# Performance work log

Measured on AMD Instinct MI355X. Metric: run time of the kernel, lower is better.

Reference implementation:

```python
import jax, jax.numpy as jnp
import numpy as np

N_NODES = 500_000
N_EDGES = 32_000_000

def setup_inputs() -> dict:
    key = jax.random.key(0)
    k1, k2, k3 = jax.random.split(key, 3)
    x = jax.random.uniform(k1, (N_NODES, 1), dtype=jnp.float32)
    edge_index = jax.random.randint(k2, (2, N_EDGES), 0, N_NODES, dtype=jnp.int32)
    edge_probs = jax.random.uniform(k3, (N_EDGES,), dtype=jnp.float32)
    edge_weight = jnp.ones((1,), dtype=jnp.float32)
    self_loop = jnp.ones((1,), dtype=jnp.float32)
    return {"x": x, "edge_index": edge_index, "edge_probs": edge_probs,
            "edge_weight": edge_weight, "self_loop": self_loop}

def reference(x, edge_index, edge_probs, edge_weight, self_loop):
    # x: (N,1), edge_index: (2,E), edge_probs: (E,)
    src = edge_index[0]
    dst = edge_index[1]
    # messages: (E,1) = 1 - x[src] * p_e * w
    messages = 1.0 - x[src] * edge_probs[:, None] * edge_weight
    # scatter-multiply into dst nodes; nodes with no incoming edges get 1
    agg = jax.ops.segment_prod(messages, dst, num_segments=x.shape[0])
    return agg + self_loop * x
```

## Files before the change

kernel.cpp:

```cpp
#include <hip/hip_runtime.h>


#if defined(__has_builtin) && __has_builtin(__builtin_amdgcn_exp2f)
#define EXP2F(v) __builtin_amdgcn_exp2f(v)
#else
#define EXP2F(v) exp2f(v)
#endif

#define BLK 256
#define NB_SHIFT 13
#define NB (1 << NB_SHIFT)
#define EPB 16384
#define MAXK 256

__device__ __forceinline__ unsigned xcc_id() {
    return __builtin_amdgcn_s_getreg((31 << 11) | 20) & 7u;
}
__device__ __forceinline__ void atomic_fadd_l2(float* p, float v) {
    asm volatile("global_atomic_add_f32 %0, %1, off" :: "v"(p), "v"(v) : "memory");
}
__device__ __forceinline__ void atomic_fadd_agent(float* p, float v) {
    unsafeAtomicAdd(p, v);
}

__global__ void init_zero(float* __restrict__ ws, int n) {
    int i = blockIdx.x * blockDim.x + threadIdx.x;
    if (i < n) ws[i] = 0.0f;
}

template <bool USE_L2>
__global__ __launch_bounds__(256) void edge_scatter(
        const float* __restrict__ x,
        const int* __restrict__ src,
        const int* __restrict__ dst,
        const float* __restrict__ probs,
        const float* __restrict__ w_ptr,
        float* __restrict__ logsum,
        int n_nodes, int n_e4) {
    const float w = w_ptr[0];
    float* ls = USE_L2 ? (logsum + (size_t)xcc_id() * (size_t)n_nodes) : logsum;
    int i = blockIdx.x * blockDim.x + threadIdx.x;
    if (i >= n_e4) return;
    int4   s = ((const int4*)src)[i];
    int4   d = ((const int4*)dst)[i];
    float4 p = ((const float4*)probs)[i];
    float m0 = __log2f(1.0f - x[s.x] * p.x * w);
    float m1 = __log2f(1.0f - x[s.y] * p.y * w);
    float m2 = __log2f(1.0f - x[s.z] * p.z * w);
    float m3 = __log2f(1.0f - x[s.w] * p.w * w);
    if (USE_L2) {
        atomic_fadd_l2(&ls[d.x], m0); atomic_fadd_l2(&ls[d.y], m1);
        atomic_fadd_l2(&ls[d.z], m2); atomic_fadd_l2(&ls[d.w], m3);
    } else {
        atomic_fadd_agent(&ls[d.x], m0); atomic_fadd_agent(&ls[d.y], m1);
        atomic_fadd_agent(&ls[d.z], m2); atomic_fadd_agent(&ls[d.w], m3);
    }
}

template <bool USE_L2>
__global__ void edge_scatter_tail(
        const float* __restrict__ x,
        const int* __restrict__ src,
        const int* __restrict__ dst,
        const float* __restrict__ probs,
        const float* __restrict__ w_ptr,
        float* __restrict__ logsum,
        int n_nodes, int start, int n_edges) {
    const float w = w_ptr[0];
    float* ls = USE_L2 ? (logsum + (size_t)xcc_id() * (size_t)n_nodes) : logsum;
    int i = start + blockIdx.x * blockDim.x + threadIdx.x;
    if (i >= n_edges) return;
    float m = __log2f(1.0f - x[src[i]] * probs[i] * w);
    if (USE_L2) atomic_fadd_l2(&ls[dst[i]], m);
    else        atomic_fadd_agent(&ls[dst[i]], m);
}

__global__ void finalize8(const float* __restrict__ x,
                          const float* __restrict__ sl_ptr,
                          const float* __restrict__ logsum,
                          float* __restrict__ out, int n) {
    int i = blockIdx.x * blockDim.x + threadIdx.x;
    if (i >= n) return;
    float s = 0.0f;
    #pragma unroll
    for (int r = 0; r < 8; ++r) s += logsum[(size_t)r * n + i];
    out[i] = EXP2F(s) + sl_ptr[0] * x[i];
}

__global__ void finalize1(const float* __restrict__ x,
                          const float* __restrict__ sl_ptr,
                          const float* __restrict__ logsum,
                          float* __restrict__ out, int n) {
    int i = blockIdx.x * blockDim.x + threadIdx.x;
    if (i < n) out[i] = EXP2F(logsum[i]) + sl_ptr[0] * x[i];
}


__global__ __launch_bounds__(256) void k_hist(
        const int* __restrict__ dstp,
        unsigned* __restrict__ hist,
        int ebase, int ecount, int K, int G0, int vec_ok) {
    __shared__ unsigned h[MAXK];
    const int b = blockIdx.x;
    const int t = threadIdx.x;
    for (int i = t; i < K; i += BLK) h[i] = 0;
    __syncthreads();
    const int begin = ebase + b * EPB;
    const int end   = min(begin + EPB, ebase + ecount);
    if (vec_ok) {
        for (int e0 = begin + t * 4; e0 < end; e0 += BLK * 4) {
            if (e0 + 4 <= end) {
                const int4 d = *(const int4*)(dstp + e0);
                atomicAdd(&h[(unsigned)d.x >> NB_SHIFT], 1u);
                atomicAdd(&h[(unsigned)d.y >> NB_SHIFT], 1u);
                atomicAdd(&h[(unsigned)d.z >> NB_SHIFT], 1u);
                atomicAdd(&h[(unsigned)d.w >> NB_SHIFT], 1u);
            } else {
                for (int e = e0; e < end; ++e)
                    atomicAdd(&h[(unsigned)dstp[e] >> NB_SHIFT], 1u);
            }
        }
    } else {
        for (int e0 = begin + t * 4; e0 < end; e0 += BLK * 4) {
            const int ee = min(e0 + 4, end);
            for (int e = e0; e < ee; ++e)
                atomicAdd(&h[(unsigned)dstp[e] >> NB_SHIFT], 1u);
        }
    }
    __syncthreads();
    for (int i = t; i < K; i += BLK) hist[(size_t)i * G0 + b] = h[i];
}

__global__ __launch_bounds__(256) void k_scan_row(
        unsigned* __restrict__ hist, unsigned* __restrict__ btot,
        int G0, int Gr) {
    __shared__ unsigned wsum[4];
    __shared__ unsigned carry;
    const int k = blockIdx.x;
    const int t = threadIdx.x;
    unsigned* row = hist + (size_t)k * G0;
    if (t == 0) carry = 0;
    __syncthreads();
    for (int c0 = 0; c0 < Gr; c0 += BLK) {
        const unsigned v = (c0 + t < Gr) ? row[c0 + t] : 0u;
        unsigned xs = v;
        #pragma unroll
        for (int o = 1; o < 64; o <<= 1) {
            const unsigned y = __shfl_up(xs, o, 64);
            if ((t & 63) >= o) xs += y;
        }
        if ((t & 63) == 63) wsum[t >> 6] = xs;
        __syncthreads();
        unsigned woff = 0;
        for (int wv = 0; wv < (t >> 6); ++wv) woff += wsum[wv];
        const unsigned ex = xs + woff - v + carry;
        if (c0 + t < Gr) row[c0 + t] = ex;
        const unsigned ctot = wsum[0] + wsum[1] + wsum[2] + wsum[3];
        __syncthreads();
        if (t == 0) carry += ctot;
        __syncthreads();
    }
    if (t == 0) btot[k] = carry;
}

__global__ __launch_bounds__(256) void k_scan_bkt(
        const unsigned* __restrict__ btot, unsigned* __restrict__ bbase, int K) {
    __shared__ unsigned wsum[4];
    const int t = threadIdx.x;
    const unsigned v = (t < K) ? btot[t] : 0u;
    unsigned xs = v;
    #pragma unroll
    for (int o = 1; o < 64; o <<= 1) {
        const unsigned y = __shfl_up(xs, o, 64);
        if ((t & 63) >= o) xs += y;
    }
    if ((t & 63) == 63) wsum[t >> 6] = xs;
    __syncthreads();
    unsigned woff = 0;
    for (int wv = 0; wv < (t >> 6); ++wv) woff += wsum[wv];
    if (t < K) bbase[t] = xs + woff - v;
}

__global__ __launch_bounds__(256) void k_scatter(
        const float* __restrict__ x,
        const int* __restrict__ src,
        const int* __restrict__ dstp,
        const float* __restrict__ probs,
        const float* __restrict__ w_ptr,
        const unsigned* __restrict__ base,
        const unsigned* __restrict__ bbase,
        uint2* __restrict__ queue,
        int ebase, int ecount, int K, int G0, int vec_ok) {
    __shared__ unsigned cur[MAXK];
    const int b = blockIdx.x;
    const int t = threadIdx.x;
    for (int i = t; i < K; i += BLK)
        cur[i] = bbase[i] + base[(size_t)i * G0 + b];
    __syncthreads();
    const float w = w_ptr[0];
    const int begin = ebase + b * EPB;
    const int end   = min(begin + EPB, ebase + ecount);
    auto one = [&](int e) {
        const int dv = dstp[e];
        const float m = __log2f(1.0f - x[src[e]] * probs[e] * w);
        const unsigned kk = (unsigned)dv >> NB_SHIFT;
        const unsigned r = atomicAdd(&cur[kk], 1u);
        queue[r] = make_uint2((unsigned)dv & (NB - 1), __float_as_uint(m));
    };
    if (vec_ok) {
        for (int e0 = begin + t * 4; e0 < end; e0 += BLK * 4) {
            if (e0 + 4 <= end) {
                const int4   d  = *(const int4*)(dstp + e0);
                const int4   sv = *(const int4*)(src + e0);
                const float4 pv = *(const float4*)(probs + e0);
                const float m0 = __log2f(1.0f - x[sv.x] * pv.x * w);
                const float m1 = __log2f(1.0f - x[sv.y] * pv.y * w);
                const float m2 = __log2f(1.0f - x[sv.z] * pv.z * w);
                const float m3 = __log2f(1.0f - x[sv.w] * pv.w * w);
                const unsigned r0 = atomicAdd(&cur[(unsigned)d.x >> NB_SHIFT], 1u);
                queue[r0] = make_uint2((unsigned)d.x & (NB - 1), __float_as_uint(m0));
                const unsigned r1 = atomicAdd(&cur[(unsigned)d.y >> NB_SHIFT], 1u);
                queue[r1] = make_uint2((unsigned)d.y & (NB - 1), __float_as_uint(m1));
                const unsigned r2 = atomicAdd(&cur[(unsigned)d.z >> NB_SHIFT], 1u);
                queue[r2] = make_uint2((unsigned)d.z & (NB - 1), __float_as_uint(m2));
                const unsigned r3 = atomicAdd(&cur[(unsigned)d.w >> NB_SHIFT], 1u);
                queue[r3] = make_uint2((unsigned)d.w & (NB - 1), __float_as_uint(m3));
            } else {
                for (int e = e0; e < end; ++e) one(e);
            }
        }
    } else {
        for (int e0 = begin + t * 4; e0 < end; e0 += BLK * 4) {
            const int ee = min(e0 + 4, end);
            for (int e = e0; e < ee; ++e) one(e);
        }
    }
}

__global__ __launch_bounds__(256) void k_accum(
        const uint2* __restrict__ queue,
        const unsigned* __restrict__ btot,
        const unsigned* __restrict__ bbase,
        float* __restrict__ partial,
        int s3, int first) {
    __shared__ float acc[NB];
    const int t = threadIdx.x;
    const int k = blockIdx.x / s3;
    const int s = blockIdx.x % s3;
    for (int i = t; i < NB; i += BLK) acc[i] = 0.0f;
    __syncthreads();
    const unsigned cnt = btot[k];
    const unsigned per = (cnt + s3 - 1) / s3;
    const unsigned lo = min((unsigned)s * per, cnt);
    const unsigned hi = min(lo + per, cnt);
    const uint2* q = queue + bbase[k];
    unsigned i = lo + t;
    for (; i + BLK < hi; i += 2 * BLK) {
        const uint2 e0 = q[i];
        const uint2 e1 = q[i + BLK];
        atomicAdd(&acc[e0.x], __uint_as_float(e0.y));
        atomicAdd(&acc[e1.x], __uint_as_float(e1.y));
    }
    for (; i < hi; i += BLK) {
        const uint2 e = q[i];
        atomicAdd(&acc[e.x], __uint_as_float(e.y));
    }
    __syncthreads();
    float* p = partial + (size_t)blockIdx.x * NB;
    if (first) { for (int j = t; j < NB; j += BLK) p[j] = acc[j]; }
    else       { for (int j = t; j < NB; j += BLK) p[j] += acc[j]; }
}

__global__ __launch_bounds__(256) void k_final(
        const float* __restrict__ x,
        const float* __restrict__ sl_ptr,
        const float* __restrict__ partial,
        float* __restrict__ out, int n, int s3) {
    int i = blockIdx.x * blockDim.x + threadIdx.x;
    if (i >= n) return;
    const int k = i >> NB_SHIFT;
    const int l = i & (NB - 1);
    const float* p = partial + ((size_t)k * s3) * NB + l;
    float ssum = 0.0f;
    for (int r = 0; r < s3; ++r) ssum += p[(size_t)r * NB];
    out[i] = EXP2F(ssum) + sl_ptr[0] * x[i];
}


static inline size_t alignup256(size_t v) { return (v + 255) & ~(size_t)255; }

extern "C" void kernel_launch(void* const* d_in, const int* in_sizes, int n_in,
                              void* d_out, int out_size, void* d_ws, size_t ws_size,
                              hipStream_t stream) {
    const float* x          = (const float*)d_in[0];
    const int*   edge_index = (const int*)  d_in[1];
    const float* probs      = (const float*)d_in[2];
    const float* w          = (const float*)d_in[3];
    const float* sl         = (const float*)d_in[4];

    const int n_nodes = in_sizes[0];
    const int n_edges = in_sizes[1] / 2;
    const int* src = edge_index;
    const int* dst = edge_index + n_edges;

    const int K = (n_nodes + NB - 1) >> NB_SHIFT;

    int R = 0, s3 = 0, G0 = 0;
    long long Er = 0;
    size_t off_hist = 0, off_btot = 0, off_bbase = 0, off_queue = 0;
    if (n_nodes > 0 && n_edges > 0 && K >= 1 && K <= MAXK) {
        const int s3cand[5] = {16, 8, 4, 2, 1};
        for (int r = 1; r <= 64 && !R; ++r) {
            long long er = (((long long)n_edges + r - 1) / r + 3) & ~3LL;
            if (er < 4) er = 4;
            int g = (int)((er + EPB - 1) / EPB);
            if (g < 1) g = 1;
            for (int ci = 0; ci < 5; ++ci) {
                const int cs3 = s3cand[ci];
                const size_t pb = (size_t)K * cs3 * NB * sizeof(float);
                const size_t hb = (size_t)K * g * sizeof(unsigned);
                const size_t kb = (size_t)K * sizeof(unsigned);
                const size_t o1 = alignup256(pb);
                const size_t o2 = o1 + alignup256(hb);
                const size_t o3 = o2 + alignup256(kb);
                const size_t o4 = o3 + alignup256(kb);
                const size_t tot = o4 + (size_t)er * sizeof(uint2);
                if (tot <= ws_size) {
                    R = r; s3 = cs3; G0 = g; Er = er;
                    off_hist = o1; off_btot = o2; off_bbase = o3; off_queue = o4;
                    break;
                }
            }
        }
    }

    if (R > 0) {
        char* wsb = (char*)d_ws;
        float*    partial_p = (float*)wsb;
        unsigned* hist_p    = (unsigned*)(wsb + off_hist);
        unsigned* btot_p    = (unsigned*)(wsb + off_btot);
        unsigned* bbase_p   = (unsigned*)(wsb + off_bbase);
        uint2*    queue_p   = (uint2*)(wsb + off_queue);

        const int vec_ok = ((n_edges & 3) == 0) ? 1 : 0;
        for (int r = 0; r < R; ++r) {
            const long long eb = (long long)r * Er;
            if (eb >= n_edges) break;
            const long long rem = (long long)n_edges - eb;
            const int ec = (int)(rem < Er ? rem : Er);
            const int g = (ec + EPB - 1) / EPB;
            k_hist<<<g, BLK, 0, stream>>>(dst, hist_p, (int)eb, ec, K, G0, vec_ok);
            k_scan_row<<<K, BLK, 0, stream>>>(hist_p, btot_p, G0, g);
            k_scan_bkt<<<1, BLK, 0, stream>>>(btot_p, bbase_p, K);
            k_scatter<<<g, BLK, 0, stream>>>(
                x, src, dst, probs, w, hist_p, bbase_p, queue_p,
                (int)eb, ec, K, G0, vec_ok);
            k_accum<<<K * s3, BLK, 0, stream>>>(
                queue_p, btot_p, bbase_p, partial_p, s3, r == 0 ? 1 : 0);
        }
        k_final<<<(n_nodes + 255) / 256, 256, 0, stream>>>(
            x, sl, partial_p, (float*)d_out, n_nodes, s3);
        return;
    }

    float* logsum = (float*)d_ws;
    const bool use_l2 = ws_size >= (size_t)8 * (size_t)n_nodes * sizeof(float);
    const int n_ls = use_l2 ? 8 * n_nodes : n_nodes;

    init_zero<<<(n_ls + 255) / 256, 256, 0, stream>>>(logsum, n_ls);

    const int e4 = n_edges / 4;
    const int tail_start = e4 * 4;
    const int tail = n_edges - tail_start;

    if (use_l2) {
        if (e4 > 0)
            edge_scatter<true><<<(e4 + 255) / 256, 256, 0, stream>>>(
                x, src, dst, probs, w, logsum, n_nodes, e4);
        if (tail > 0)
            edge_scatter_tail<true><<<(tail + 255) / 256, 256, 0, stream>>>(
                x, src, dst, probs, w, logsum, n_nodes, tail_start, n_edges);
        finalize8<<<(n_nodes + 255) / 256, 256, 0, stream>>>(
            x, sl, logsum, (float*)d_out, n_nodes);
    } else {
        if (e4 > 0)
            edge_scatter<false><<<(e4 + 255) / 256, 256, 0, stream>>>(
                x, src, dst, probs, w, logsum, n_nodes, e4);
        if (tail > 0)
            edge_scatter_tail<false><<<(tail + 255) / 256, 256, 0, stream>>>(
                x, src, dst, probs, w, logsum, n_nodes, tail_start, n_edges);
        finalize1<<<(n_nodes + 255) / 256, 256, 0, stream>>>(
            x, sl, logsum, (float*)d_out, n_nodes);
    }
}
```

Before: 972.7 us.

## Stage scatter bucketing in LDS and write coalesced runs to the queue

The scatter kernel now sorts each block's edges by bucket in a shared-memory staging buffer, then writes them to the global queue in contiguous runs per bucket, found by binary search over per-block bucket offsets. This replaces scattered 8-byte global writes with coalesced ones. Edges per block drop from 16384 to 4096 so the 32KB stage fits in LDS, which means more blocks and a larger histogram. Bucket bases are padded to even sizes so the accumulate kernel can read entries two at a time with 16-byte loads, and the workspace reserves extra padding for this.

```diff
diff --git a/kernel.cpp b/kernel.cpp
--- a/kernel.cpp
+++ b/kernel.cpp
@@ -10,7 +10,7 @@
 #define BLK 256
 #define NB_SHIFT 13
 #define NB (1 << NB_SHIFT)
-#define EPB 16384
+#define EPB 4096
 #define MAXK 256
 
 __device__ __forceinline__ unsigned xcc_id() {
@@ -167,7 +167,7 @@
         const unsigned* __restrict__ btot, unsigned* __restrict__ bbase, int K) {
     __shared__ unsigned wsum[4];
     const int t = threadIdx.x;
-    const unsigned v = (t < K) ? btot[t] : 0u;
+    const unsigned v = (t < K) ? ((btot[t] + 1u) & ~1u) : 0u;
     unsigned xs = v;
     #pragma unroll
     for (int o = 1; o < 64; o <<= 1) {
@@ -188,15 +188,45 @@
         const float* __restrict__ probs,
         const float* __restrict__ w_ptr,
         const unsigned* __restrict__ base,
+        const unsigned* __restrict__ btot,
         const unsigned* __restrict__ bbase,
         uint2* __restrict__ queue,
-        int ebase, int ecount, int K, int G0, int vec_ok) {
-    __shared__ unsigned cur[MAXK];
+        int ebase, int ecount, int K, int G0, int Gr, int vec_ok) {
+    __shared__ uint2    stage[EPB];
+    __shared__ unsigned off_s[MAXK + 1];
+    __shared__ unsigned cur_s[MAXK];
+    __shared__ unsigned gb2_s[MAXK];
+    __shared__ unsigned wsum[4];
     const int b = blockIdx.x;
     const int t = threadIdx.x;
-    for (int i = t; i < K; i += BLK)
-        cur[i] = bbase[i] + base[(size_t)i * G0 + b];
-    __syncthreads();
+    if (K <= 0) return;
+
+    unsigned v = 0, gbeg = 0;
+    if (t < K) {
+        const unsigned cme = base[(size_t)t * G0 + b];
+        const unsigned cnx = (b + 1 < Gr) ? base[(size_t)t * G0 + b + 1] : btot[t];
+        v = cnx - cme;
+        gbeg = bbase[t] + cme;
+    }
+    unsigned xs = v;
+    #pragma unroll
+    for (int o = 1; o < 64; o <<= 1) {
+        const unsigned y = __shfl_up(xs, o, 64);
+        if ((t & 63) >= o) xs += y;
+    }
+    if ((t & 63) == 63) wsum[t >> 6] = xs;
+    __syncthreads();
+    unsigned woff = 0;
+    for (int wv = 0; wv < (t >> 6); ++wv) woff += wsum[wv];
+    const unsigned ex = xs + woff - v;
+    if (t < K) {
+        off_s[t] = ex;
+        cur_s[t] = ex;
+        gb2_s[t] = gbeg - ex;
+    }
+    if (t == 0) off_s[K] = wsum[0] + wsum[1] + wsum[2] + wsum[3];
+    __syncthreads();
+
     const float w = w_ptr[0];
     const int begin = ebase + b * EPB;
     const int end   = min(begin + EPB, ebase + ecount);
@@ -204,8 +234,8 @@
         const int dv = dstp[e];
         const float m = __log2f(1.0f - x[src[e]] * probs[e] * w);
         const unsigned kk = (unsigned)dv >> NB_SHIFT;
-        const unsigned r = atomicAdd(&cur[kk], 1u);
-        queue[r] = make_uint2((unsigned)dv & (NB - 1), __float_as_uint(m));
+        const unsigned r = atomicAdd(&cur_s[kk], 1u);
+        stage[r] = make_uint2((unsigned)dv & (NB - 1), __float_as_uint(m));
     };
     if (vec_ok) {
         for (int e0 = begin + t * 4; e0 < end; e0 += BLK * 4) {
@@ -217,14 +247,14 @@
                 const float m1 = __log2f(1.0f - x[sv.y] * pv.y * w);
                 const float m2 = __log2f(1.0f - x[sv.z] * pv.z * w);
                 const float m3 = __log2f(1.0f - x[sv.w] * pv.w * w);
-                const unsigned r0 = atomicAdd(&cur[(unsigned)d.x >> NB_SHIFT], 1u);
-                queue[r0] = make_uint2((unsigned)d.x & (NB - 1), __float_as_uint(m0));
-                const unsigned r1 = atomicAdd(&cur[(unsigned)d.y >> NB_SHIFT], 1u);
-                queue[r1] = make_uint2((unsigned)d.y & (NB - 1), __float_as_uint(m1));
-                const unsigned r2 = atomicAdd(&cur[(unsigned)d.z >> NB_SHIFT], 1u);
-                queue[r2] = make_uint2((unsigned)d.z & (NB - 1), __float_as_uint(m2));
-                const unsigned r3 = atomicAdd(&cur[(unsigned)d.w >> NB_SHIFT], 1u);
-                queue[r3] = make_uint2((unsigned)d.w & (NB - 1), __float_as_uint(m3));
+                const unsigned r0 = atomicAdd(&cur_s[(unsigned)d.x >> NB_SHIFT], 1u);
+                stage[r0] = make_uint2((unsigned)d.x & (NB - 1), __float_as_uint(m0));
+                const unsigned r1 = atomicAdd(&cur_s[(unsigned)d.y >> NB_SHIFT], 1u);
+                stage[r1] = make_uint2((unsigned)d.y & (NB - 1), __float_as_uint(m1));
+                const unsigned r2 = atomicAdd(&cur_s[(unsigned)d.z >> NB_SHIFT], 1u);
+                stage[r2] = make_uint2((unsigned)d.z & (NB - 1), __float_as_uint(m2));
+                const unsigned r3 = atomicAdd(&cur_s[(unsigned)d.w >> NB_SHIFT], 1u);
+                stage[r3] = make_uint2((unsigned)d.w & (NB - 1), __float_as_uint(m3));
             } else {
                 for (int e = e0; e < end; ++e) one(e);
             }
@@ -234,6 +264,18 @@
             const int ee = min(e0 + 4, end);
             for (int e = e0; e < ee; ++e) one(e);
         }
+    }
+    __syncthreads();
+
+    const int total = end - begin;
+    for (int j = t; j < total; j += BLK) {
+        const uint2 e = stage[j];
+        int lo = 0, hi = K;
+        while (hi - lo > 1) {
+            const int mid = (lo + hi) >> 1;
+            if ((unsigned)j >= off_s[mid]) lo = mid; else hi = mid;
+        }
+        queue[(size_t)gb2_s[lo] + (unsigned)j] = e;
     }
 }
 
@@ -250,19 +292,21 @@
     for (int i = t; i < NB; i += BLK) acc[i] = 0.0f;
     __syncthreads();
     const unsigned cnt = btot[k];
-    const unsigned per = (cnt + s3 - 1) / s3;
+    unsigned per = (cnt + s3 - 1) / s3;
+    per = (per + 1u) & ~1u;
     const unsigned lo = min((unsigned)s * per, cnt);
     const unsigned hi = min(lo + per, cnt);
-    const uint2* q = queue + bbase[k];
-    unsigned i = lo + t;
-    for (; i + BLK < hi; i += 2 * BLK) {
-        const uint2 e0 = q[i];
-        const uint2 e1 = q[i + BLK];
-        atomicAdd(&acc[e0.x], __uint_as_float(e0.y));
-        atomicAdd(&acc[e1.x], __uint_as_float(e1.y));
-    }
-    for (; i < hi; i += BLK) {
-        const uint2 e = q[i];
+    const unsigned n = hi - lo;
+    const uint2* q = queue + bbase[k] + lo;
+    const uint4* q4 = (const uint4*)q;
+    const unsigned n4 = n >> 1;
+    for (unsigned p = t; p < n4; p += BLK) {
+        const uint4 e = q4[p];
+        atomicAdd(&acc[e.x], __uint_as_float(e.y));
+        atomicAdd(&acc[e.z], __uint_as_float(e.w));
+    }
+    if ((n & 1u) && t == 0) {
+        const uint2 e = q[n - 1];
         atomicAdd(&acc[e.x], __uint_as_float(e.y));
     }
     __syncthreads();
@@ -324,7 +368,7 @@
                 const size_t o2 = o1 + alignup256(hb);
                 const size_t o3 = o2 + alignup256(kb);
                 const size_t o4 = o3 + alignup256(kb);
-                const size_t tot = o4 + (size_t)er * sizeof(uint2);
+                const size_t tot = o4 + ((size_t)er + 2 * MAXK) * sizeof(uint2);
                 if (tot <= ws_size) {
                     R = r; s3 = cs3; G0 = g; Er = er;
                     off_hist = o1; off_btot = o2; off_bbase = o3; off_queue = o4;
@@ -353,8 +397,8 @@
             k_scan_row<<<K, BLK, 0, stream>>>(hist_p, btot_p, G0, g);
             k_scan_bkt<<<1, BLK, 0, stream>>>(btot_p, bbase_p, K);
             k_scatter<<<g, BLK, 0, stream>>>(
-                x, src, dst, probs, w, hist_p, bbase_p, queue_p,
-                (int)eb, ec, K, G0, vec_ok);
+                x, src, dst, probs, w, hist_p, btot_p, bbase_p, queue_p,
+                (int)eb, ec, K, G0, g, vec_ok);
             k_accum<<<K * s3, BLK, 0, stream>>>(
                 queue_p, btot_p, bbase_p, partial_p, s3, r == 0 ? 1 : 0);
         }
```

New measurement: 861.0 us. -11.5%, faster.
